# Kernel optimization log

Hardware: AMD Instinct MI355X
Metric: run time of the kernel (lower is better)

## Reference

```python
import jax, jax.numpy as jnp
import numpy as np

B, L, D = 4, 816, 2048
SEP = 768            # gemma (image+text) prefix length
P_LEN = 3            # proprio tokens inside the action-expert block
N, K, H = 8, 1, 256  # heads, kv heads (GQA), head dim
G = N // K
GEMMA_MLP, ACTION_MLP = 16384, 4096
SOFTCAP = 50.0
BIG_NEG = -2.3819763e38


def rms_norm(x, scale, eps=1e-6):
    var = jnp.mean(jnp.square(x.astype(jnp.float32)), axis=-1, keepdims=True)
    normed = x * jax.lax.rsqrt(var + eps)
    return (normed * (1.0 + scale)).astype(x.dtype)


def apply_rope(x, positions, max_wavelength=10_000):
    # x: [B, T, n, H], positions: [B, T]
    head_dim = x.shape[-1]
    freq_exp = (2.0 / head_dim) * jnp.arange(head_dim // 2, dtype=jnp.float32)
    timescale = max_wavelength ** freq_exp
    radians = positions[..., None].astype(jnp.float32) / timescale[None, None, :]
    radians = radians[..., None, :]  # [B, T, 1, H/2]
    sin, cos = jnp.sin(radians), jnp.cos(radians)
    x1, x2 = jnp.split(x, 2, axis=-1)
    return jnp.concatenate([x1 * cos - x2 * sin, x2 * cos + x1 * sin], axis=-1).astype(x.dtype)


def get_qkv(xn, positions, wq, wkv):
    # wq: [N, D, H], wkv: [2, K, D, H]
    q = jnp.einsum('btd,ndh->btnh', xn, wq)
    k = jnp.einsum('bsd,kdh->bskh', xn, wkv[0])
    v = jnp.einsum('bsd,kdh->bskh', xn, wkv[1])
    q = apply_rope(q, positions) * (H ** -0.5)  # query_pre_attn_norm='rsqrt_head_dim'
    k = apply_rope(k, positions)
    return q, k, v


def geglu_ffn(x, w_gating, w_linear):
    # gemma GeGLU: w_gating [2, D, hidden], w_linear [hidden, D]
    gate = jax.nn.gelu(jnp.einsum('btd,dh->bth', x, w_gating[0]))
    act = gate * jnp.einsum('btd,dh->bth', x, w_gating[1])
    return jnp.einsum('bth,hd->btd', act, w_linear)


def setup_inputs() -> dict:
    key = jax.random.key(0)
    ks = jax.random.split(key, 16)
    s = 0.02
    x = jax.random.normal(ks[0], (B, L, D), jnp.float32)
    positions = jnp.broadcast_to(jnp.arange(L, dtype=jnp.int32), (B, L))
    # PiZero block mask: full attention within gemma prefix; proprio and action
    # blocks attend to everything before them plus themselves (mask_ar cumsum trick).
    mask_ar = np.zeros(L, dtype=np.int64)
    mask_ar[SEP] = 1
    mask_ar[SEP + P_LEN] = 1
    cm = np.cumsum(mask_ar)
    attn = cm[None, :] <= cm[:, None]  # [L_q, L_kv]
    attn_mask = jnp.asarray(np.broadcast_to(attn[None, None], (B, 1, L, L)))
    return {
        'x': x,
        'positions': positions,
        'attn_mask': attn_mask,
        'separation_idx': SEP,
        'pre_attn_scale': jnp.zeros((D,), jnp.float32),
        'pre_ffw_scale': jnp.zeros((D,), jnp.float32),
        'gq_w': jax.random.normal(ks[1], (N, D, H), jnp.float32) * s,
        'gkv_w': jax.random.normal(ks[2], (2, K, D, H), jnp.float32) * s,
        'go_w': jax.random.normal(ks[3], (N, H, D), jnp.float32) * s,
        'aq_w': jax.random.normal(ks[4], (N, D, H), jnp.float32) * s,
        'akv_w': jax.random.normal(ks[5], (2, K, D, H), jnp.float32) * s,
        'ao_w': jax.random.normal(ks[6], (N, H, D), jnp.float32) * s,
        'g_gating': jax.random.normal(ks[7], (2, D, GEMMA_MLP), jnp.float32) * s,
        'g_linear': jax.random.normal(ks[8], (GEMMA_MLP, D), jnp.float32) * s,
        'a_gating': jax.random.normal(ks[9], (2, D, ACTION_MLP), jnp.float32) * s,
        'a_linear': jax.random.normal(ks[10], (ACTION_MLP, D), jnp.float32) * s,
    }


def reference(x, positions, attn_mask, separation_idx, pre_attn_scale, pre_ffw_scale,
              gq_w, gkv_w, go_w, aq_w, akv_w, ao_w,
              g_gating, g_linear, a_gating, a_linear):
    sep = separation_idx
    xg, xa = x[:, :sep, :], x[:, sep:, :]
    # shared pre-attention RMSNorm applied to both expert streams
    ng = rms_norm(xg, pre_attn_scale)
    na = rms_norm(xa, pre_attn_scale)
    pg, pa = positions[:, :sep], positions[:, sep:]
    qg, kg, vg = get_qkv(ng, pg, gq_w, gkv_w)
    qa, ka, va = get_qkv(na, pa, aq_w, akv_w)
    # joint attention over concatenated streams
    q = jnp.concatenate([qg, qa], axis=1)   # [B, L, N, H]
    k = jnp.concatenate([kg, ka], axis=1)   # [B, L, K, H]
    v = jnp.concatenate([vg, va], axis=1)
    Bq, T = q.shape[0], q.shape[1]
    qr = q.reshape(Bq, T, K, G, H)
    logits = jnp.einsum('btkgh,bskh->bkgts', qr, k)
    logits = jnp.tanh(logits / SOFTCAP) * SOFTCAP  # attn logit softcap
    logits = jnp.where(attn_mask[:, :, None, :, :], logits, BIG_NEG)
    probs = jax.nn.softmax(logits.astype(jnp.float32), axis=-1).astype(logits.dtype)
    attn_out = jnp.einsum('bkgts,bskh->btkgh', probs, v).reshape(Bq, T, N, H)
    # per-expert output projections
    og = jnp.einsum('btnh,nhd->btd', attn_out[:, :sep], go_w)
    oa = jnp.einsum('btnh,nhd->btd', attn_out[:, sep:], ao_w)

    def post(attn_o, res, gating, lin):
        # faithful to source: final residual is mlp(norm(attn+res)) + res
        h = rms_norm(attn_o + res, pre_ffw_scale)
        return geglu_ffn(h, gating, lin) + res

    yg = post(og, xg, g_gating, g_linear)
    ya = post(oa, xa, a_gating, a_linear)
    return jnp.concatenate([yg, ya], axis=1)
```

## Files before the change

### kernel.cpp

```cpp
#include <hip/hip_runtime.h>
#include <hip/hip_bf16.h>

typedef __bf16 bfx8 __attribute__((ext_vector_type(8)));
typedef __bf16 bfx4 __attribute__((ext_vector_type(4)));
typedef float f32x4 __attribute__((ext_vector_type(4)));

#define MFMA16(a, b, c) __builtin_amdgcn_mfma_f32_16x16x32_bf16((a), (b), (c), 0, 0, 0)

__device__ __forceinline__ void gl_lds16(const __bf16* g, __bf16* l) {
  __builtin_amdgcn_global_load_lds(
      (const __attribute__((address_space(1))) unsigned int*)(const void*)g,
      (__attribute__((address_space(3))) unsigned int*)(void*)l, 16, 0, 0);
}

__device__ __forceinline__ unsigned pack_bf2(float a, float b) {
  unsigned short ua = __builtin_bit_cast(unsigned short, (__bf16)a);
  unsigned short ub = __builtin_bit_cast(unsigned short, (__bf16)b);
  return (unsigned)ua | ((unsigned)ub << 16);
}

__device__ __forceinline__ float gelu_tanh_f(float x) {
  float u = 0.7978845608028654f * (x + 0.044715f * x * x * x);
  float t;
  if (u > 10.f) t = 1.f;
  else if (u < -10.f) t = -1.f;
  else { float e = __expf(2.f * u); t = (e - 1.f) / (e + 1.f); }
  return 0.5f * x * (1.f + t);
}

__global__ __launch_bounds__(256)
void rmsnorm_kernel(const float* __restrict__ X, const float* __restrict__ X2,
                    const float* __restrict__ scale, __bf16* __restrict__ out) {
  __shared__ float wsum[4];
  const int row = blockIdx.x, tid = threadIdx.x;
  const size_t base = (size_t)row * 2048;
  f32x4 v[2];
  float ss = 0.f;
#pragma unroll
  for (int i = 0; i < 2; ++i) {
    const int idx = tid * 4 + i * 1024;
    v[i] = *(const f32x4*)(X + base + idx);
    if (X2) { f32x4 u = *(const f32x4*)(X2 + base + idx); v[i] = v[i] + u; }
#pragma unroll
    for (int j = 0; j < 4; ++j) ss += v[i][j] * v[i][j];
  }
#pragma unroll
  for (int o = 32; o > 0; o >>= 1) ss += __shfl_xor(ss, o, 64);
  if ((tid & 63) == 0) wsum[tid >> 6] = ss;
  __syncthreads();
  const float tot = wsum[0] + wsum[1] + wsum[2] + wsum[3];
  const float rs = rsqrtf(tot * (1.f / 2048.f) + 1e-6f);
#pragma unroll
  for (int i = 0; i < 2; ++i) {
    const int idx = tid * 4 + i * 1024;
    f32x4 sc = *(const f32x4*)(scale + idx);
    bfx4 ov;
#pragma unroll
    for (int j = 0; j < 4; ++j) ov[j] = (__bf16)(v[i][j] * rs * (1.f + sc[j]));
    *(bfx4*)(out + base + idx) = ov;
  }
}

__global__ __launch_bounds__(256)
void rope_bf_kernel(__bf16* __restrict__ buf, const int* __restrict__ pos,
                    int nheads, int rstride, float outscale) {
  const int row = blockIdx.x;
  const float p = (float)pos[row];
  const int total = nheads * 128;
  const size_t rbase = (size_t)row * (size_t)rstride;
  for (int idx = threadIdx.x; idx < total; idx += 256) {
    const int n = idx >> 7, i = idx & 127;
    const float ts = __expf(-(float)i * 0.071955784f);
    float sn, cs;
    __sincosf(p * ts, &sn, &cs);
    __bf16* bp = buf + rbase + n * 256 + i;
    const float x1 = (float)bp[0], x2 = (float)bp[128];
    bp[0]   = (__bf16)((x1 * cs - x2 * sn) * outscale);
    bp[128] = (__bf16)((x2 * cs + x1 * sn) * outscale);
  }
}

__global__ __launch_bounds__(256)
void rope_kernel(const float* __restrict__ in, const int* __restrict__ pos,
                 __bf16* __restrict__ outp, int nheads, float outscale) {
  const int row = blockIdx.x;
  const float p = (float)pos[row];
  const int total = nheads * 128;
  const size_t rbase = (size_t)row * (size_t)(nheads * 256);
  for (int idx = threadIdx.x; idx < total; idx += 256) {
    const int n = idx >> 7, i = idx & 127;
    const float ts = __expf(-(float)i * 0.071955784f);
    float sn, cs;
    __sincosf(p * ts, &sn, &cs);
    const float* bp = in + rbase + n * 256 + i;
    const float x1 = bp[0], x2 = bp[128];
    __bf16* ob = outp + rbase + n * 256 + i;
    ob[0]   = (__bf16)((x1 * cs - x2 * sn) * outscale);
    ob[128] = (__bf16)((x2 * cs + x1 * sn) * outscale);
  }
}

__global__ __launch_bounds__(256)
void convw_kernel(const float* __restrict__ in, __bf16* __restrict__ out,
                  int K, int headDim) {
  __shared__ __bf16 tile[64][65];
  const int tc0 = blockIdx.x * 64;
  const int tk0 = blockIdx.y * 64;
  const int tid = threadIdx.x;
  const int cchunk = tid & 15, krow = tid >> 4;
  const int c = tc0 + cchunk * 4;
  const float* colbase = in + (size_t)(c / headDim) * (size_t)K * headDim + (c % headDim);
#pragma unroll
  for (int i = 0; i < 4; ++i) {
    const int k = tk0 + krow + i * 16;
    f32x4 v = *(const f32x4*)(colbase + (size_t)k * headDim);
#pragma unroll
    for (int j = 0; j < 4; ++j) tile[cchunk * 4 + j][krow + i * 16] = (__bf16)v[j];
  }
  __syncthreads();
  const int nks = K >> 5;
#pragma unroll
  for (int s = 0; s < 2; ++s) {
    const int ch = tid + s * 256;
    const int wc = ch >> 3, wk8 = (ch & 7) * 8;
    bfx8 v;
#pragma unroll
    for (int j = 0; j < 8; ++j) v[j] = tile[wc][wk8 + j];
    const int col = tc0 + wc;
    const int kchunk = (tk0 + wk8) >> 3;
    const int cp = col >> 7, m = col & 127;
    const int ks = kchunk >> 2, lg = kchunk & 3;
    const int p = lg ^ ((m >> 1) & 3);
    *(bfx8*)(out + ((size_t)(cp * nks + ks)) * 4096 + m * 32 + p * 8) = v;
  }
}

__global__ __launch_bounds__(512, 2)
void ffn_dual256(const __bf16* __restrict__ A, const __bf16* __restrict__ Wg,
                 const __bf16* __restrict__ Wa, __bf16* __restrict__ C,
                 int Mpb, int lda, int strideA, int Kd,
                 int ldc, int strideC, int mbPerBatch) {
  __shared__ __align__(16) __bf16 As[2 * 2 * 8192];
  __shared__ __align__(16) __bf16 Bs[2 * 2 * 8192];
  const int tid = threadIdx.x;
  const int lane = tid & 63;
  const int wid = tid >> 6;
  const int wr = wid >> 2;
  const int wc = wid & 3;
  const int qi = lane & 15, g = lane >> 4;
  const int b = blockIdx.x / mbPerBatch;
  const int row0 = (blockIdx.x % mbPerBatch) * 256;
  const int col0 = blockIdx.y * 128;
  const __bf16* Ab = A + (size_t)b * strideA;
  const size_t nks = (size_t)(Kd >> 5);
  const __bf16* Bgp = Wg + ((size_t)(col0 >> 7)) * nks * 4096;
  const __bf16* Bap = Wa + ((size_t)(col0 >> 7)) * nks * 4096;
  const int NT = Kd >> 6;

  const int sm = tid >> 2, sp = tid & 3;
  const int slg = sp ^ ((sm >> 1) & 3);
  int r0 = row0 + sm;       if (r0 >= Mpb) r0 = Mpb - 1;
  int r1 = row0 + 128 + sm; if (r1 >= Mpb) r1 = Mpb - 1;
  const __bf16* asrc0 = Ab + (size_t)r0 * lda + slg * 8;
  const __bf16* asrc1 = Ab + (size_t)r1 * lda + slg * 8;

  auto stage_half = [&](int gh) {
    if (gh >= 4 * NT) return;
    const int t = gh >> 2, which = gh & 3;
    const int bufi = t & 1;
    if ((which & 1) == 0) {
      const int h = which >> 1;
      __bf16* dst = &As[bufi * 16384 + h * 8192];
      const __bf16* src = (h ? asrc1 : asrc0) + t * 64;
      gl_lds16(src, dst + tid * 8);
      gl_lds16(src + 32, dst + 4096 + tid * 8);
    } else {
      const int pan = which >> 1;
      __bf16* dst = &Bs[bufi * 16384 + pan * 8192];
      const __bf16* src = (pan ? Bap : Bgp) + (size_t)(t * 2) * 4096 + tid * 8;
      gl_lds16(src, dst + tid * 8);
      gl_lds16(src + 4096, dst + 4096 + tid * 8);
    }
  };

  f32x4 acc[2][2][4][2];
#pragma unroll
  for (int a0 = 0; a0 < 2; ++a0)
#pragma unroll
    for (int a1 = 0; a1 < 2; ++a1)
#pragma unroll
      for (int a2 = 0; a2 < 4; ++a2)
#pragma unroll
        for (int a3 = 0; a3 < 2; ++a3) acc[a0][a1][a2][a3] = f32x4{0.f, 0.f, 0.f, 0.f};

  for (int gh = 0; gh < 6; ++gh) stage_half(gh);
  asm volatile("s_waitcnt vmcnt(4)" ::: "memory");
  __builtin_amdgcn_s_barrier();
  asm volatile("" ::: "memory");

  for (int t = 0; t < NT; ++t) {
    const int cb = (t & 1) * 16384;
    bfx8 af[4][2], bf[2][2][2];

#pragma unroll
    for (int mi = 0; mi < 4; ++mi) {
      const int m = wr * 64 + mi * 16 + qi;
      const int sl = g ^ ((m >> 1) & 3);
      const int ba = cb + m * 32 + sl * 8;
      af[mi][0] = *(const bfx8*)(&As[ba]);
      af[mi][1] = *(const bfx8*)(&As[ba + 4096]);
    }
#pragma unroll
    for (int pan = 0; pan < 2; ++pan)
#pragma unroll
      for (int ni = 0; ni < 2; ++ni) {
        const int m = wc * 32 + ni * 16 + qi;
        const int sl = g ^ ((m >> 1) & 3);
        const int bb = cb + pan * 8192 + m * 32 + sl * 8;
        bf[pan][ni][0] = *(const bfx8*)(&Bs[bb]);
        bf[pan][ni][1] = *(const bfx8*)(&Bs[bb + 4096]);
      }
    stage_half(4 * t + 6);
    stage_half(4 * t + 7);
    __builtin_amdgcn_s_barrier();
    asm volatile("s_waitcnt lgkmcnt(0)" ::: "memory");
    __builtin_amdgcn_sched_barrier(0);
    __builtin_amdgcn_s_setprio(1);
#pragma unroll
    for (int pan = 0; pan < 2; ++pan)
#pragma unroll
      for (int mi = 0; mi < 4; ++mi)
#pragma unroll
        for (int ni = 0; ni < 2; ++ni) {
          acc[0][pan][mi][ni] = MFMA16(af[mi][0], bf[pan][ni][0], acc[0][pan][mi][ni]);
          acc[0][pan][mi][ni] = MFMA16(af[mi][1], bf[pan][ni][1], acc[0][pan][mi][ni]);
        }
    __builtin_amdgcn_s_setprio(0);
    __builtin_amdgcn_s_barrier();
    asm volatile("" ::: "memory");

#pragma unroll
    for (int mi = 0; mi < 4; ++mi) {
      const int m = wr * 64 + mi * 16 + qi;
      const int sl = g ^ ((m >> 1) & 3);
      const int ba = cb + 8192 + m * 32 + sl * 8;
      af[mi][0] = *(const bfx8*)(&As[ba]);
      af[mi][1] = *(const bfx8*)(&As[ba + 4096]);
    }
    stage_half(4 * t + 8);
    stage_half(4 * t + 9);
    if (t + 2 < NT) asm volatile("s_waitcnt vmcnt(4)" ::: "memory");
    else            asm volatile("s_waitcnt vmcnt(0)" ::: "memory");
    __builtin_amdgcn_s_barrier();
    asm volatile("s_waitcnt lgkmcnt(0)" ::: "memory");
    __builtin_amdgcn_sched_barrier(0);
    __builtin_amdgcn_s_setprio(1);
#pragma unroll
    for (int pan = 0; pan < 2; ++pan)
#pragma unroll
      for (int mi = 0; mi < 4; ++mi)
#pragma unroll
        for (int ni = 0; ni < 2; ++ni) {
          acc[1][pan][mi][ni] = MFMA16(af[mi][0], bf[pan][ni][0], acc[1][pan][mi][ni]);
          acc[1][pan][mi][ni] = MFMA16(af[mi][1], bf[pan][ni][1], acc[1][pan][mi][ni]);
        }
    __builtin_amdgcn_s_setprio(0);
    __builtin_amdgcn_s_barrier();
    asm volatile("" ::: "memory");
  }

#pragma unroll
  for (int mh = 0; mh < 2; ++mh)
#pragma unroll
    for (int mi = 0; mi < 4; ++mi)
#pragma unroll
      for (int ni = 0; ni < 2; ++ni) {
        const int col = col0 + wc * 32 + ni * 16 + qi;
#pragma unroll
        for (int r = 0; r < 4; ++r) {
          const int row = row0 + mh * 128 + wr * 64 + mi * 16 + g * 4 + r;
          if (row >= Mpb) continue;
          C[(size_t)b * strideC + (size_t)row * ldc + col] =
              (__bf16)(gelu_tanh_f(acc[mh][0][mi][ni][r]) * acc[mh][1][mi][ni][r]);
        }
      }
}

__global__ __launch_bounds__(256, 2)
void gemm_bt2(const __bf16* __restrict__ A, const __bf16* __restrict__ Bt,
              void* __restrict__ C, void* __restrict__ C2, const void* __restrict__ Extra,
              int Mpb, int lda, int strideA, int Kd,
              int ldc, int strideC, int mbPerBatch,
              int outMode, int ldct) {
  __shared__ __align__(16) __bf16 As[2][8192];
  __shared__ __align__(16) __bf16 Bs[2][8192];
  const int tid = threadIdx.x;
  const int lane = tid & 63;
  const int wid = tid >> 6;
  const int b = blockIdx.x / mbPerBatch;
  const int row0 = (blockIdx.x % mbPerBatch) * 128;
  const int col0 = blockIdx.y * 128;
  const __bf16* Ab = A + (size_t)b * strideA;
  const size_t nks = (size_t)(Kd >> 5);
  const __bf16* Bpan0 = Bt + ((size_t)(col0 >> 7)) * nks * 4096;
  const int wm = (wid >> 1) * 64, wn = (wid & 1) * 64;
  const int qi = lane & 15, g = lane >> 4;

  const int m0 = tid >> 2, p0 = tid & 3;
  const int lg0 = p0 ^ ((m0 >> 1) & 3);
  const int m1 = m0 + 64;
  const int lg1 = p0 ^ ((m1 >> 1) & 3);
  int mr0 = row0 + m0; if (mr0 >= Mpb) mr0 = Mpb - 1;
  int mr1 = row0 + m1; if (mr1 >= Mpb) mr1 = Mpb - 1;
  const __bf16* asrc0 = Ab + (size_t)mr0 * lda + lg0 * 8;
  const __bf16* asrc1 = Ab + (size_t)mr1 * lda + lg1 * 8;
  const int nt = Kd >> 6;

  auto stage = [&](int t, int bufi) {
    const int k0 = t * 64;
    gl_lds16(asrc0 + k0, &As[bufi][tid * 8]);
    gl_lds16(asrc1 + k0, &As[bufi][(tid + 256) * 8]);
    gl_lds16(asrc0 + k0 + 32, &As[bufi][4096 + tid * 8]);
    gl_lds16(asrc1 + k0 + 32, &As[bufi][4096 + (tid + 256) * 8]);
    const __bf16* pb = Bpan0 + (size_t)(k0 >> 5) * 4096;
    gl_lds16(pb + tid * 8, &Bs[bufi][tid * 8]);
    gl_lds16(pb + (tid + 256) * 8, &Bs[bufi][(tid + 256) * 8]);
    gl_lds16(pb + 4096 + tid * 8, &Bs[bufi][4096 + tid * 8]);
    gl_lds16(pb + 4096 + (tid + 256) * 8, &Bs[bufi][4096 + (tid + 256) * 8]);
  };

  f32x4 acc[4][4];
#pragma unroll
  for (int i = 0; i < 4; ++i)
#pragma unroll
    for (int j = 0; j < 4; ++j) acc[i][j] = f32x4{0.f, 0.f, 0.f, 0.f};

  stage(0, 0);
  if (nt > 1) stage(1, 1);

  for (int t = 0; t < nt; ++t) {
    const int cur = t & 1;
    if (t + 1 < nt) asm volatile("s_waitcnt vmcnt(8)" ::: "memory");
    else            asm volatile("s_waitcnt vmcnt(0)" ::: "memory");
    __builtin_amdgcn_s_barrier();
    asm volatile("" ::: "memory");
#pragma unroll
    for (int ks = 0; ks < 2; ++ks) {
      bfx8 af[4], bf[4];
#pragma unroll
      for (int mi = 0; mi < 4; ++mi) {
        const int m = wm + mi * 16 + qi;
        const int sl = g ^ ((m >> 1) & 3);
        af[mi] = *(const bfx8*)(&As[cur][ks * 4096 + m * 32 + sl * 8]);
      }
#pragma unroll
      for (int ni = 0; ni < 4; ++ni) {
        const int n = wn + ni * 16 + qi;
        const int sl = g ^ ((n >> 1) & 3);
        bf[ni] = *(const bfx8*)(&Bs[cur][ks * 4096 + n * 32 + sl * 8]);
      }
#pragma unroll
      for (int mi = 0; mi < 4; ++mi)
#pragma unroll
        for (int ni = 0; ni < 4; ++ni)
          acc[mi][ni] = MFMA16(af[mi], bf[ni], acc[mi][ni]);
    }
    asm volatile("s_waitcnt lgkmcnt(0)" ::: "memory");
    __builtin_amdgcn_s_barrier();
    asm volatile("" ::: "memory");
    if (t + 2 < nt) stage(t + 2, cur);
  }

#pragma unroll
  for (int mi = 0; mi < 4; ++mi) {
#pragma unroll
    for (int ni = 0; ni < 4; ++ni) {
      const int col = col0 + wn + ni * 16 + qi;
      if (outMode == 5 && col >= 2304) {
        const int vcol = col - 2304;
        const int rowb = row0 + wm + mi * 16 + g * 4;
        if (rowb < Mpb) {
          bfx4 ov;
#pragma unroll
          for (int r = 0; r < 4; ++r) ov[r] = (__bf16)acc[mi][ni][r];
          *(bfx4*)((__bf16*)C2 + (size_t)b * (256 * 816) + (size_t)vcol * 816 + rowb) = ov;
        }
        continue;
      }
#pragma unroll
      for (int r = 0; r < 4; ++r) {
        const int row = row0 + wm + mi * 16 + g * 4 + r;
        if (row >= Mpb) continue;
        const float v = acc[mi][ni][r];
        if (outMode == 0) {
          ((float*)C)[(size_t)b * strideC + (size_t)row * ldc + col] = v;
        } else if (outMode == 1 || outMode == 5) {
          ((__bf16*)C)[(size_t)b * strideC + (size_t)row * ldc + col] = (__bf16)v;
        } else {
          const size_t ix = (size_t)b * strideC + (size_t)row * ldc + col;
          ((float*)C)[ix] = v + ((const float*)Extra)[ix];
        }
      }
    }
  }
  (void)ldct;
}

__global__ __launch_bounds__(256, 2)
void ffn_dual(const __bf16* __restrict__ A, const __bf16* __restrict__ Wg,
              const __bf16* __restrict__ Wa, __bf16* __restrict__ C,
              int Mpb, int lda, int strideA, int Kd,
              int ldc, int strideC, int mbPerBatch) {
  __shared__ __align__(16) __bf16 As[2][8192];
  __shared__ __align__(16) __bf16 Bs[2][8192];
  const int tid = threadIdx.x;
  const int lane = tid & 63;
  const int wid = tid >> 6;
  const int b = blockIdx.x / mbPerBatch;
  const int row0 = (blockIdx.x % mbPerBatch) * 128;
  const int col0 = blockIdx.y * 128;
  const __bf16* Ab = A + (size_t)b * strideA;
  const size_t nks = (size_t)(Kd >> 5);
  const int wm = (wid >> 1) * 64, wn = (wid & 1) * 64;
  const int qi = lane & 15, g = lane >> 4;

  const int m0 = tid >> 2, p0 = tid & 3;
  const int lg0 = p0 ^ ((m0 >> 1) & 3);
  const int m1 = m0 + 64;
  const int lg1 = p0 ^ ((m1 >> 1) & 3);
  int mr0 = row0 + m0; if (mr0 >= Mpb) mr0 = Mpb - 1;
  int mr1 = row0 + m1; if (mr1 >= Mpb) mr1 = Mpb - 1;
  const __bf16* asrc0 = Ab + (size_t)mr0 * lda + lg0 * 8;
  const __bf16* asrc1 = Ab + (size_t)mr1 * lda + lg1 * 8;
  const int nt = Kd >> 6;

  f32x4 gval[4][4];
  f32x4 acc[4][4];

// ... 193 lines not shown
  const int qt = blockIdx.x, hn = blockIdx.y, b = blockIdx.z;
  const int q0 = qt * 64;
  const int qi = lane & 15, g = lane >> 4;

  int qrow = q0 + wid * 16 + qi;
  if (qrow > 815) qrow = 815;
  const int cmq = (qrow >= 768) + (qrow >= 771);
  const __bf16* qrp = qp + (size_t)(b * 816 + qrow) * qstride + hn * 256 + g * 8;
  bfx8 qf[8];
#pragma unroll
  for (int kf = 0; kf < 8; ++kf) qf[kf] = *(const bfx8*)(qrp + kf * 32);

  f32x4 oacc[16];
#pragma unroll
  for (int i = 0; i < 16; ++i) oacc[i] = f32x4{0.f, 0.f, 0.f, 0.f};
  float den = 0.f;

  const int ntiles = (q0 + 63 < 768) ? 12 : 13;
  for (int t = 0; t < ntiles; ++t) {
    const int kv0 = t * 64;
#pragma unroll
    for (int mi = 0; mi < 4; ++mi) {
      f32x4 sac = f32x4{0.f, 0.f, 0.f, 0.f};
      int srow = kv0 + mi * 16 + qi;
      if (srow > 815) srow = 815;
      const __bf16* kp = kp0 + (size_t)(b * 816 + srow) * kstride + g * 8;
#pragma unroll
      for (int kf = 0; kf < 8; ++kf) {
        bfx8 a = *(const bfx8*)(kp + kf * 32);
        sac = MFMA16(a, qf[kf], sac);
      }
      float pv[4];
#pragma unroll
      for (int r = 0; r < 4; ++r) {
        const int s = kv0 + mi * 16 + g * 4 + r;
        const float l = sac[r];
        const float e2 = __expf(l * 0.04f);
        const float capped = 50.f * (e2 - 1.f) / (e2 + 1.f);
        const int cms = (s >= 768) + (s >= 771);
        const bool ok = (s < 816) && (cms <= cmq);
        const float p = ok ? __expf(capped) : 0.f;
        den += p;
        pv[r] = p;
      }
      const unsigned lo = pack_bf2(pv[0], pv[1]);
      const unsigned hi = pack_bf2(pv[2], pv[3]);
      const int slot = 2 * mi + (g >> 1);
      const int phys = slot ^ (qi & 7);
      char* pb = (char*)&Ps[wid][0] + qi * 128 + phys * 16 + (g & 1) * 8;
      *(unsigned*)(pb) = lo;
      *(unsigned*)(pb + 4) = hi;
    }
    asm volatile("s_waitcnt lgkmcnt(0)" ::: "memory");
    bfx8 pa[2];
#pragma unroll
    for (int k2 = 0; k2 < 2; ++k2) {
      const int sl = (k2 * 4 + g) ^ (qi & 7);
      pa[k2] = *(const bfx8*)((const char*)&Ps[wid][0] + qi * 128 + sl * 16);
    }
#pragma unroll
    for (int hf = 0; hf < 16; ++hf) {
      const int h = hf * 16 + qi;
#pragma unroll
      for (int k2 = 0; k2 < 2; ++k2) {
        int s0 = kv0 + k2 * 32 + g * 8;
        if (s0 > 808) s0 = 808;
        bfx8 vb = *(const bfx8*)(vt + ((size_t)(b * 256 + h)) * 816 + s0);
        oacc[hf] = MFMA16(pa[k2], vb, oacc[hf]);
      }
    }
    asm volatile("s_waitcnt lgkmcnt(0)" ::: "memory");
  }

  den += __shfl_xor(den, 16, 64);
  den += __shfl_xor(den, 32, 64);
  if (lane < 16) denw[wid][qi] = den;
  asm volatile("s_waitcnt lgkmcnt(0)" ::: "memory");
#pragma unroll
  for (int r = 0; r < 4; ++r) {
    const int qg = q0 + wid * 16 + g * 4 + r;
    if (qg >= 816) continue;
    const float di = 1.f / denw[wid][g * 4 + r];
#pragma unroll
    for (int hf = 0; hf < 16; ++hf) {
      ao[((size_t)(b * 816 + qg)) * 2048 + hn * 256 + hf * 16 + qi] =
          (__bf16)(oacc[hf][r] * di);
    }
  }
}

extern "C" void kernel_launch(void* const* d_in, const int* in_sizes, int n_in,
                              void* d_out, int out_size, void* d_ws, size_t ws_size,
                              hipStream_t stream) {
  (void)in_sizes; (void)n_in; (void)out_size;
  const float* x      = (const float*)d_in[0];
  const int*   pos    = (const int*)d_in[1];
  const float* s_attn = (const float*)d_in[4];
  const float* s_ffw  = (const float*)d_in[5];
  const float* gq     = (const float*)d_in[6];
  const float* gkv    = (const float*)d_in[7];
  const float* go     = (const float*)d_in[8];
  const float* aq     = (const float*)d_in[9];
  const float* akv    = (const float*)d_in[10];
  const float* aow    = (const float*)d_in[11];
  const float* gg     = (const float*)d_in[12];
  const float* gl     = (const float*)d_in[13];
  const float* ag     = (const float*)d_in[14];
  const float* al     = (const float*)d_in[15];
  float* outp = (float*)d_out;
  char* ws = (char*)d_ws;
  dim3 blk(256);

  const size_t NEED_BATCH = 577437696u;
  const size_t NEED_FAST  = 423297024u;

  if (ws_size >= NEED_FAST) {
    const bool batched = (ws_size >= NEED_BATCH);
    __bf16* wQKVg = (__bf16*)(ws + 0);
    __bf16* wQKVa = (__bf16*)(ws + 10485760);
    __bf16* goT = (__bf16*)(ws + 20971520);
    __bf16* aoT = (__bf16*)(ws + 29360128);
    __bf16* ggT = (__bf16*)(ws + 37748736);
    __bf16* glT = (__bf16*)(ws + 171966464);
    __bf16* agT = (__bf16*)(ws + 239075328);
    __bf16* alT = (__bf16*)(ws + 272629760);
    __bf16* xn   = (__bf16*)(ws + 289406976);
    __bf16* qkb  = (__bf16*)(ws + 302776320);
    __bf16* vt   = (__bf16*)(ws + 317816832);
    __bf16* aob  = (__bf16*)(ws + 319488000);
    float*  ob   = (float*)(ws + 332857344);
    __bf16* hb   = (__bf16*)(ws + 359596032);
    __bf16* gate  = (__bf16*)(ws + 372965376);
    __bf16* act   = (__bf16*)(ws + 398131200);
    __bf16* act4  = (__bf16*)(ws + 473628672);
    __bf16* actA4 = (__bf16*)(ws + 575864832);

    convw_kernel<<<dim3(32, 32), blk, 0, stream>>>(gq, wQKVg, 2048, 256);
    convw_kernel<<<dim3(4, 32), blk, 0, stream>>>(gkv, wQKVg + 16 * 64 * 4096, 2048, 256);
    convw_kernel<<<dim3(4, 32), blk, 0, stream>>>(gkv + 2048 * 256, wQKVg + 18 * 64 * 4096, 2048, 256);
    convw_kernel<<<dim3(32, 32), blk, 0, stream>>>(aq, wQKVa, 2048, 256);
    convw_kernel<<<dim3(4, 32), blk, 0, stream>>>(akv, wQKVa + 16 * 64 * 4096, 2048, 256);
    convw_kernel<<<dim3(4, 32), blk, 0, stream>>>(akv + 2048 * 256, wQKVa + 18 * 64 * 4096, 2048, 256);
    convw_kernel<<<dim3(32, 32), blk, 0, stream>>>(go, goT, 2048, 2048);
    convw_kernel<<<dim3(32, 32), blk, 0, stream>>>(aow, aoT, 2048, 2048);
    convw_kernel<<<dim3(256, 32), blk, 0, stream>>>(gg, ggT, 2048, 16384);
    convw_kernel<<<dim3(256, 32), blk, 0, stream>>>(gg + (size_t)2048 * 16384, ggT + (size_t)16384 * 2048, 2048, 16384);
    convw_kernel<<<dim3(32, 256), blk, 0, stream>>>(gl, glT, 16384, 2048);
    convw_kernel<<<dim3(64, 32), blk, 0, stream>>>(ag, agT, 2048, 4096);
    convw_kernel<<<dim3(64, 32), blk, 0, stream>>>(ag + (size_t)2048 * 4096, agT + (size_t)4096 * 2048, 2048, 4096);
    convw_kernel<<<dim3(32, 64), blk, 0, stream>>>(al, alT, 4096, 2048);

    rmsnorm_kernel<<<3264, blk, 0, stream>>>(x, nullptr, s_attn, xn);

    gemm_bt2<<<dim3(24, 20), blk, 0, stream>>>(xn, wQKVg, qkb, vt, nullptr,
        768, 2048, 816 * 2048, 2048, 2304, 816 * 2304, 6, 5, 0);
    gemm_bt2<<<dim3(4, 20), blk, 0, stream>>>(xn + 768 * 2048, wQKVa, qkb + 768 * 2304, vt + 768, nullptr,
        48, 2048, 816 * 2048, 2048, 2304, 816 * 2304, 1, 5, 0);

    rope_bf_kernel<<<3264, blk, 0, stream>>>(qkb, pos, 8, 2304, 0.0625f);
    rope_bf_kernel<<<3264, blk, 0, stream>>>(qkb + 2048, pos, 1, 2304, 1.0f);

    attn_kernel<<<dim3(13, 8, 4), blk, 0, stream>>>(qkb, qkb + 2048, vt, aob, 2304, 2304);

    gemm_bt2<<<dim3(24, 16), blk, 0, stream>>>(aob, goT, ob, nullptr, nullptr,
        768, 2048, 816 * 2048, 2048, 2048, 816 * 2048, 6, 0, 0);
    gemm_bt2<<<dim3(4, 16), blk, 0, stream>>>(aob + 768 * 2048, aoT, ob + 768 * 2048, nullptr, nullptr,
        48, 2048, 816 * 2048, 2048, 2048, 816 * 2048, 1, 0, 0);

    rmsnorm_kernel<<<3264, blk, 0, stream>>>(ob, x, s_ffw, hb);

    if (batched) {
      ffn_dual256<<<dim3(12, 128), dim3(512), 0, stream>>>(hb, ggT, ggT + (size_t)16384 * 2048, act4,
          768, 2048, 816 * 2048, 2048, 16384, 768 * 16384, 3);
      gemm_bt2<<<dim3(24, 16), blk, 0, stream>>>(act4, glT, outp, nullptr, x,
          768, 16384, 768 * 16384, 16384, 2048, 816 * 2048, 6, 2, 0);
      ffn_dual<<<dim3(4, 32), blk, 0, stream>>>(hb + 768 * 2048, agT, agT + (size_t)4096 * 2048, actA4,
          48, 2048, 816 * 2048, 2048, 4096, 48 * 4096, 1);
      gemm_bt2<<<dim3(4, 16), blk, 0, stream>>>(actA4, alT, outp + 768 * 2048, nullptr, x + 768 * 2048,
          48, 4096, 48 * 4096, 4096, 2048, 816 * 2048, 1, 2, 0);
    } else {
      for (int bb = 0; bb < 4; ++bb) {
        const __bf16* hg = hb + (size_t)bb * 816 * 2048;
        float* og = outp + (size_t)bb * 816 * 2048;
        const float* xg = x + (size_t)bb * 816 * 2048;
        ffn_dual<<<dim3(6, 128), blk, 0, stream>>>(hg, ggT, ggT + (size_t)16384 * 2048, act,
            768, 2048, 0, 2048, 16384, 0, 6);
        gemm_bt2<<<dim3(6, 16), blk, 0, stream>>>(act, glT, og, nullptr, xg,
            768, 16384, 0, 16384, 2048, 0, 6, 2, 0);
        const __bf16* ha = hg + 768 * 2048;
        ffn_dual<<<dim3(1, 32), blk, 0, stream>>>(ha, agT, agT + (size_t)4096 * 2048, gate,
            48, 2048, 0, 2048, 4096, 0, 1);
        gemm_bt2<<<dim3(1, 16), blk, 0, stream>>>(gate, alT, og + 768 * 2048, nullptr, xg + 768 * 2048,
            48, 4096, 0, 4096, 2048, 0, 1, 2, 0);
      }
    }
    return;
  }

  if (ws_size < 164000000u) return;
  __bf16* xn   = (__bf16*)(ws + 0);
  float*  qf   = (float*)(ws + 13369344);
  __bf16* qbb  = (__bf16*)(ws + 40108032);
  float*  kf   = (float*)(ws + 53477376);
  __bf16* kbb  = (__bf16*)(ws + 56819712);
  __bf16* vt   = (__bf16*)(ws + 58490880);
  __bf16* aob  = (__bf16*)(ws + 60162048);
  float*  ob   = (float*)(ws + 73531392);
  __bf16* hb   = (__bf16*)(ws + 100270080);
  __bf16* gate = (__bf16*)(ws + 113639424);
  __bf16* act  = (__bf16*)(ws + 138805248);

  rmsnorm_kernel<<<3264, blk, 0, stream>>>(x, nullptr, s_attn, xn);
  gemm_kernel<<<dim3(24, 16), blk, 0, stream>>>(xn, gq, qf, nullptr,
      768, 2048, 816 * 2048, 256, 256, 2048, 2048, 816 * 2048, 6, 0, 0);
  gemm_kernel<<<dim3(4, 16), blk, 0, stream>>>(xn + 768 * 2048, aq, qf + 768 * 2048, nullptr,
      48, 2048, 816 * 2048, 256, 256, 2048, 2048, 816 * 2048, 1, 0, 0);
  gemm_kernel<<<dim3(24, 2), blk, 0, stream>>>(xn, gkv, kf, nullptr,
      768, 2048, 816 * 2048, 256, 256, 2048, 256, 816 * 256, 6, 0, 0);
  gemm_kernel<<<dim3(4, 2), blk, 0, stream>>>(xn + 768 * 2048, akv, kf + 768 * 256, nullptr,
      48, 2048, 816 * 2048, 256, 256, 2048, 256, 816 * 256, 1, 0, 0);
  gemm_kernel<<<dim3(24, 2), blk, 0, stream>>>(xn, gkv + 2048 * 256, vt, nullptr,
      768, 2048, 816 * 2048, 256, 256, 2048, 0, 256 * 816, 6, 3, 816);
  gemm_kernel<<<dim3(4, 2), blk, 0, stream>>>(xn + 768 * 2048, akv + 2048 * 256, vt + 768, nullptr,
      48, 2048, 816 * 2048, 256, 256, 2048, 0, 256 * 816, 1, 3, 816);
  rope_kernel<<<3264, blk, 0, stream>>>(qf, pos, qbb, 8, 0.0625f);
  rope_kernel<<<3264, blk, 0, stream>>>(kf, pos, kbb, 1, 1.0f);
  attn_kernel<<<dim3(13, 8, 4), blk, 0, stream>>>(qbb, kbb, vt, aob, 2048, 256);
  gemm_kernel<<<dim3(24, 16), blk, 0, stream>>>(aob, go, ob, nullptr,
      768, 2048, 816 * 2048, 2048, 0, 2048, 2048, 816 * 2048, 6, 0, 0);
  gemm_kernel<<<dim3(4, 16), blk, 0, stream>>>(aob + 768 * 2048, aow, ob + 768 * 2048, nullptr,
      48, 2048, 816 * 2048, 2048, 0, 2048, 2048, 816 * 2048, 1, 0, 0);
  rmsnorm_kernel<<<3264, blk, 0, stream>>>(ob, x, s_ffw, hb);
  for (int bb = 0; bb < 4; ++bb) {
    const __bf16* hg = hb + (size_t)bb * 816 * 2048;
    float* og = outp + (size_t)bb * 816 * 2048;
    const float* xg = x + (size_t)bb * 816 * 2048;
    gemm_kernel<<<dim3(6, 128), blk, 0, stream>>>(hg, gg, gate, nullptr,
        768, 2048, 0, 16384, 0, 2048, 16384, 0, 6, 1, 0);
    gemm_kernel<<<dim3(6, 128), blk, 0, stream>>>(hg, gg + 2048 * 16384, act, gate,
        768, 2048, 0, 16384, 0, 2048, 16384, 0, 6, 4, 0);
    gemm_kernel<<<dim3(6, 16), blk, 0, stream>>>(act, gl, og, xg,
        768, 16384, 0, 2048, 0, 16384, 2048, 0, 6, 2, 0);
    const __bf16* ha = hg + 768 * 2048;
    gemm_kernel<<<dim3(1, 32), blk, 0, stream>>>(ha, ag, gate, nullptr,
        48, 2048, 0, 4096, 0, 2048, 4096, 0, 1, 1, 0);
    gemm_kernel<<<dim3(1, 32), blk, 0, stream>>>(ha, ag + 2048 * 4096, act, gate,
        48, 2048, 0, 4096, 0, 2048, 4096, 0, 1, 4, 0);
    gemm_kernel<<<dim3(1, 16), blk, 0, stream>>>(act, al, og + 768 * 2048, xg + 768 * 2048,
        48, 4096, 0, 2048, 0, 4096, 2048, 0, 1, 2, 0);
  }
}
```

Measured before the change: 1.423 ms.

## Add 256x128-tile 512-thread GEMM for large projections and XCD-aware block remap

Adds a gemm256 kernel with 256-row by 128-column tiles and 8 waves. It is used for the gemma QKV, output projection and down-projection GEMMs, so each B tile is reused across twice as many rows. Both gemm256 and ffn_dual256 remap workgroup ids in groups of 8 so that neighbouring tiles share an XCD and its L2. The cost is fewer workgroups (for example 192 on the output projection), which may underfill the CUs, and the loads are staged in finer pieces.

New measurement: 1.409 ms, median of 3. No clear change (-1.0%).

```diff
diff --git a/kernel.cpp b/kernel.cpp
--- a/kernel.cpp
+++ b/kernel.cpp
@@ -148,9 +148,13 @@
   const int wr = wid >> 2;
   const int wc = wid & 3;
   const int qi = lane & 15, g = lane >> 4;
-  const int b = blockIdx.x / mbPerBatch;
-  const int row0 = (blockIdx.x % mbPerBatch) * 256;
-  const int col0 = blockIdx.y * 128;
+  int bid = blockIdx.y * gridDim.x + blockIdx.x;
+  const int nwg = gridDim.x * gridDim.y;
+  if ((nwg & 7) == 0) bid = (bid & 7) * (nwg >> 3) + (bid >> 3);
+  const int bx = bid % gridDim.x, by = bid / gridDim.x;
+  const int b = bx / mbPerBatch;
+  const int row0 = (bx % mbPerBatch) * 256;
+  const int col0 = by * 128;
   const __bf16* Ab = A + (size_t)b * strideA;
   const size_t nks = (size_t)(Kd >> 5);
   const __bf16* Bgp = Wg + ((size_t)(col0 >> 7)) * nks * 4096;
@@ -282,6 +286,169 @@
           if (row >= Mpb) continue;
           C[(size_t)b * strideC + (size_t)row * ldc + col] =
               (__bf16)(gelu_tanh_f(acc[mh][0][mi][ni][r]) * acc[mh][1][mi][ni][r]);
+        }
+      }
+}
+
+__global__ __launch_bounds__(512, 2)
+void gemm256(const __bf16* __restrict__ A, const __bf16* __restrict__ Bt,
+             void* __restrict__ C, void* __restrict__ C2, const void* __restrict__ Extra,
+             int Mpb, int lda, int strideA, int Kd,
+             int ldc, int strideC, int mbPerBatch, int outMode) {
+  __shared__ __align__(16) __bf16 As[2 * 2 * 8192];
+  __shared__ __align__(16) __bf16 Bs[2 * 8192];
+  const int tid = threadIdx.x;
+  const int lane = tid & 63;
+  const int wid = tid >> 6;
+  const int wr = wid >> 2;
+  const int wc = wid & 3;
+  const int qi = lane & 15, g = lane >> 4;
+  int bid = blockIdx.y * gridDim.x + blockIdx.x;
+  const int nwg = gridDim.x * gridDim.y;
+  if ((nwg & 7) == 0) bid = (bid & 7) * (nwg >> 3) + (bid >> 3);
+  const int bx = bid % gridDim.x, by = bid / gridDim.x;
+  const int b = bx / mbPerBatch;
+  const int row0 = (bx % mbPerBatch) * 256;
+  const int col0 = by * 128;
+  const __bf16* Ab = A + (size_t)b * strideA;
+  const size_t nks = (size_t)(Kd >> 5);
+  const __bf16* Bp = Bt + ((size_t)(col0 >> 7)) * nks * 4096;
+  const int NT = Kd >> 6;
+
+  const int sm = tid >> 2, sp = tid & 3;
+  const int slg = sp ^ ((sm >> 1) & 3);
+  int r0 = row0 + sm;       if (r0 >= Mpb) r0 = Mpb - 1;
+  int r1 = row0 + 128 + sm; if (r1 >= Mpb) r1 = Mpb - 1;
+  const __bf16* asrc0 = Ab + (size_t)r0 * lda + slg * 8;
+  const __bf16* asrc1 = Ab + (size_t)r1 * lda + slg * 8;
+
+  auto stage_half = [&](int gh) {
+    if (gh >= 3 * NT) return;
+    const int t = gh / 3, which = gh - 3 * t;
+    const int bufi = t & 1;
+    if (which == 1) {
+      __bf16* dst = &Bs[bufi * 8192];
+      const __bf16* src = Bp + (size_t)(t * 2) * 4096 + tid * 8;
+      gl_lds16(src, dst + tid * 8);
+      gl_lds16(src + 4096, dst + 4096 + tid * 8);
+    } else {
+      const int h = which >> 1;
+      __bf16* dst = &As[bufi * 16384 + h * 8192];
+      const __bf16* src = (h ? asrc1 : asrc0) + t * 64;
+      gl_lds16(src, dst + tid * 8);
+      gl_lds16(src + 32, dst + 4096 + tid * 8);
+    }
+  };
+
+  f32x4 acc[2][4][2];
+#pragma unroll
+  for (int a0 = 0; a0 < 2; ++a0)
+#pragma unroll
+    for (int a2 = 0; a2 < 4; ++a2)
+#pragma unroll
+      for (int a3 = 0; a3 < 2; ++a3) acc[a0][a2][a3] = f32x4{0.f, 0.f, 0.f, 0.f};
+
+  for (int gh = 0; gh < 5; ++gh) stage_half(gh);
+  asm volatile("s_waitcnt vmcnt(4)" ::: "memory");
+  __builtin_amdgcn_s_barrier();
+  asm volatile("" ::: "memory");
+
+  for (int t = 0; t < NT; ++t) {
+    const int cb = (t & 1) * 16384;
+    const int cbB = (t & 1) * 8192;
+    bfx8 af[4][2], bf[2][2];
+
+#pragma unroll
+    for (int mi = 0; mi < 4; ++mi) {
+      const int m = wr * 64 + mi * 16 + qi;
+      const int sl = g ^ ((m >> 1) & 3);
+      const int ba = cb + m * 32 + sl * 8;
+      af[mi][0] = *(const bfx8*)(&As[ba]);
+      af[mi][1] = *(const bfx8*)(&As[ba + 4096]);
+    }
+#pragma unroll
+    for (int ni = 0; ni < 2; ++ni) {
+      const int m = wc * 32 + ni * 16 + qi;
+      const int sl = g ^ ((m >> 1) & 3);
+      const int bb = cbB + m * 32 + sl * 8;
+      bf[ni][0] = *(const bfx8*)(&Bs[bb]);
+      bf[ni][1] = *(const bfx8*)(&Bs[bb + 4096]);
+    }
+    stage_half(3 * t + 5);
+    __builtin_amdgcn_s_barrier();
+    asm volatile("s_waitcnt lgkmcnt(0)" ::: "memory");
+    __builtin_amdgcn_sched_barrier(0);
+    __builtin_amdgcn_s_setprio(1);
+#pragma unroll
+    for (int mi = 0; mi < 4; ++mi)
+#pragma unroll
+      for (int ni = 0; ni < 2; ++ni) {
+        acc[0][mi][ni] = MFMA16(af[mi][0], bf[ni][0], acc[0][mi][ni]);
+        acc[0][mi][ni] = MFMA16(af[mi][1], bf[ni][1], acc[0][mi][ni]);
+      }
+    __builtin_amdgcn_s_setprio(0);
+    __builtin_amdgcn_s_barrier();
+    asm volatile("" ::: "memory");
+
+#pragma unroll
+    for (int mi = 0; mi < 4; ++mi) {
+      const int m = wr * 64 + mi * 16 + qi;
+      const int sl = g ^ ((m >> 1) & 3);
+      const int ba = cb + 8192 + m * 32 + sl * 8;
+      af[mi][0] = *(const bfx8*)(&As[ba]);
+      af[mi][1] = *(const bfx8*)(&As[ba + 4096]);
+    }
+    stage_half(3 * t + 6);
+    stage_half(3 * t + 7);
+    if (t + 2 < NT) asm volatile("s_waitcnt vmcnt(4)" ::: "memory");
+    else            asm volatile("s_waitcnt vmcnt(0)" ::: "memory");
+    __builtin_amdgcn_s_barrier();
+    asm volatile("s_waitcnt lgkmcnt(0)" ::: "memory");
+    __builtin_amdgcn_sched_barrier(0);
+    __builtin_amdgcn_s_setprio(1);
+#pragma unroll
+    for (int mi = 0; mi < 4; ++mi)
+#pragma unroll
+      for (int ni = 0; ni < 2; ++ni) {
+        acc[1][mi][ni] = MFMA16(af[mi][0], bf[ni][0], acc[1][mi][ni]);
+        acc[1][mi][ni] = MFMA16(af[mi][1], bf[ni][1], acc[1][mi][ni]);
+      }
+    __builtin_amdgcn_s_setprio(0);
+    __builtin_amdgcn_s_barrier();
+    asm volatile("" ::: "memory");
+  }
+
+#pragma unroll
+  for (int mh = 0; mh < 2; ++mh)
+#pragma unroll
+    for (int mi = 0; mi < 4; ++mi)
+#pragma unroll
+      for (int ni = 0; ni < 2; ++ni) {
+        const int col = col0 + wc * 32 + ni * 16 + qi;
+        if (outMode == 5 && col >= 2304) {
+          const int vcol = col - 2304;
+          const int rowb = row0 + mh * 128 + wr * 64 + mi * 16 + g * 4;
+          if (rowb < Mpb) {
+            bfx4 ov;
+#pragma unroll
+            for (int r = 0; r < 4; ++r) ov[r] = (__bf16)acc[mh][mi][ni][r];
+            *(bfx4*)((__bf16*)C2 + (size_t)b * (256 * 816) + (size_t)vcol * 816 + rowb) = ov;
+          }
+          continue;
+        }
+#pragma unroll
+        for (int r = 0; r < 4; ++r) {
+          const int row = row0 + mh * 128 + wr * 64 + mi * 16 + g * 4 + r;
+          if (row >= Mpb) continue;
+          const float v = acc[mh][mi][ni][r];
+          if (outMode == 0) {
+            ((float*)C)[(size_t)b * strideC + (size_t)row * ldc + col] = v;
+          } else if (outMode == 5) {
+            ((__bf16*)C)[(size_t)b * strideC + (size_t)row * ldc + col] = (__bf16)v;
+          } else {
+            const size_t ix = (size_t)b * strideC + (size_t)row * ldc + col;
+            ((float*)C)[ix] = v + ((const float*)Extra)[ix];
+          }
         }
       }
 }
@@ -783,8 +950,8 @@
 
     rmsnorm_kernel<<<3264, blk, 0, stream>>>(x, nullptr, s_attn, xn);
 
-    gemm_bt2<<<dim3(24, 20), blk, 0, stream>>>(xn, wQKVg, qkb, vt, nullptr,
-        768, 2048, 816 * 2048, 2048, 2304, 816 * 2304, 6, 5, 0);
+    gemm256<<<dim3(12, 20), dim3(512), 0, stream>>>(xn, wQKVg, qkb, vt, nullptr,
+        768, 2048, 816 * 2048, 2048, 2304, 816 * 2304, 3, 5);
     gemm_bt2<<<dim3(4, 20), blk, 0, stream>>>(xn + 768 * 2048, wQKVa, qkb + 768 * 2304, vt + 768, nullptr,
         48, 2048, 816 * 2048, 2048, 2304, 816 * 2304, 1, 5, 0);
 
@@ -793,8 +960,8 @@
 
     attn_kernel<<<dim3(13, 8, 4), blk, 0, stream>>>(qkb, qkb + 2048, vt, aob, 2304, 2304);
 
-    gemm_bt2<<<dim3(24, 16), blk, 0, stream>>>(aob, goT, ob, nullptr, nullptr,
-        768, 2048, 816 * 2048, 2048, 2048, 816 * 2048, 6, 0, 0);
+    gemm256<<<dim3(12, 16), dim3(512), 0, stream>>>(aob, goT, ob, nullptr, nullptr,
+        768, 2048, 816 * 2048, 2048, 2048, 816 * 2048, 3, 0);
     gemm_bt2<<<dim3(4, 16), blk, 0, stream>>>(aob + 768 * 2048, aoT, ob + 768 * 2048, nullptr, nullptr,
         48, 2048, 816 * 2048, 2048, 2048, 816 * 2048, 1, 0, 0);
 
@@ -803,8 +970,8 @@
     if (batched) {
       ffn_dual256<<<dim3(12, 128), dim3(512), 0, stream>>>(hb, ggT, ggT + (size_t)16384 * 2048, act4,
           768, 2048, 816 * 2048, 2048, 16384, 768 * 16384, 3);
-      gemm_bt2<<<dim3(24, 16), blk, 0, stream>>>(act4, glT, outp, nullptr, x,
-          768, 16384, 768 * 16384, 16384, 2048, 816 * 2048, 6, 2, 0);
+      gemm256<<<dim3(12, 16), dim3(512), 0, stream>>>(act4, glT, outp, nullptr, x,
+          768, 16384, 768 * 16384, 16384, 2048, 816 * 2048, 3, 2);
       ffn_dual<<<dim3(4, 32), blk, 0, stream>>>(hb + 768 * 2048, agT, agT + (size_t)4096 * 2048, actA4,
           48, 2048, 816 * 2048, 2048, 4096, 48 * 4096, 1);
       gemm_bt2<<<dim3(4, 16), blk, 0, stream>>>(actA4, alT, outp + 768 * 2048, nullptr, x + 768 * 2048,
```

## Generalize 256x256 dual-panel kernel to QKV, out-proj and FFN-down GEMMs

Applied to the files above, without the earlier changes.

The FFN gate/up kernel is turned into a general dual-panel kernel with a 256x256 output tile made of two adjacent 128-column panels. Its epilogue gains output modes for plain fp32, fp32 plus residual, and bf16 with a transposed V store. The gemma QKV, attention-output and FFN-down projections now use it instead of the 128x128 gemm_bt2, which raises data reuse per block. It also adds a block-index remap that groups blocks in strides of eight. The trade-off is far fewer blocks (for example 96 or 120) on a many-CU GPU, which may leave compute units idle.

New measurement: 1.554 ms. +9.2%, slower.

```diff
diff --git a/kernel.cpp b/kernel.cpp
--- a/kernel.cpp
+++ b/kernel.cpp
@@ -136,10 +136,11 @@
 }
 
 __global__ __launch_bounds__(512, 2)
-void ffn_dual256(const __bf16* __restrict__ A, const __bf16* __restrict__ Wg,
-                 const __bf16* __restrict__ Wa, __bf16* __restrict__ C,
-                 int Mpb, int lda, int strideA, int Kd,
-                 int ldc, int strideC, int mbPerBatch) {
+void dual256(const __bf16* __restrict__ A, const __bf16* __restrict__ W0,
+             const __bf16* __restrict__ W1, void* __restrict__ C,
+             void* __restrict__ C2, const void* __restrict__ Extra,
+             int Mpb, int lda, int strideA, int Kd,
+             int ldc, int strideC, int mbPerBatch, int outMode) {
   __shared__ __align__(16) __bf16 As[2 * 2 * 8192];
   __shared__ __align__(16) __bf16 Bs[2 * 2 * 8192];
   const int tid = threadIdx.x;
@@ -148,13 +149,18 @@
   const int wr = wid >> 2;
   const int wc = wid & 3;
   const int qi = lane & 15, g = lane >> 4;
-  const int b = blockIdx.x / mbPerBatch;
-  const int row0 = (blockIdx.x % mbPerBatch) * 256;
-  const int col0 = blockIdx.y * 128;
+  int bid = blockIdx.y * gridDim.x + blockIdx.x;
+  const int nwg = gridDim.x * gridDim.y;
+  if ((nwg & 7) == 0) bid = (bid & 7) * (nwg >> 3) + (bid >> 3);
+  const int bx = bid % gridDim.x, by = bid / gridDim.x;
+  const int b = bx / mbPerBatch;
+  const int row0 = (bx % mbPerBatch) * 256;
+  const int colw = (outMode == 4) ? 128 : 256;
+  const int col0 = by * colw;
   const __bf16* Ab = A + (size_t)b * strideA;
   const size_t nks = (size_t)(Kd >> 5);
-  const __bf16* Bgp = Wg + ((size_t)(col0 >> 7)) * nks * 4096;
-  const __bf16* Bap = Wa + ((size_t)(col0 >> 7)) * nks * 4096;
+  const __bf16* Bgp = W0 + ((size_t)(col0 >> 7)) * nks * 4096;
+  const __bf16* Bap = W1 + ((size_t)(col0 >> 7)) * nks * 4096;
   const int NT = Kd >> 6;
 
   const int sm = tid >> 2, sp = tid & 3;
@@ -269,21 +275,59 @@
     asm volatile("" ::: "memory");
   }
 
-#pragma unroll
-  for (int mh = 0; mh < 2; ++mh)
-#pragma unroll
-    for (int mi = 0; mi < 4; ++mi)
-#pragma unroll
-      for (int ni = 0; ni < 2; ++ni) {
-        const int col = col0 + wc * 32 + ni * 16 + qi;
-#pragma unroll
-        for (int r = 0; r < 4; ++r) {
-          const int row = row0 + mh * 128 + wr * 64 + mi * 16 + g * 4 + r;
-          if (row >= Mpb) continue;
-          C[(size_t)b * strideC + (size_t)row * ldc + col] =
-              (__bf16)(gelu_tanh_f(acc[mh][0][mi][ni][r]) * acc[mh][1][mi][ni][r]);
+  if (outMode == 4) {
+#pragma unroll
+    for (int mh = 0; mh < 2; ++mh)
+#pragma unroll
+      for (int mi = 0; mi < 4; ++mi)
+#pragma unroll
+        for (int ni = 0; ni < 2; ++ni) {
+          const int col = col0 + wc * 32 + ni * 16 + qi;
+#pragma unroll
+          for (int r = 0; r < 4; ++r) {
+            const int row = row0 + mh * 128 + wr * 64 + mi * 16 + g * 4 + r;
+            if (row >= Mpb) continue;
+            ((__bf16*)C)[(size_t)b * strideC + (size_t)row * ldc + col] =
+                (__bf16)(gelu_tanh_f(acc[mh][0][mi][ni][r]) * acc[mh][1][mi][ni][r]);
+          }
         }
-      }
+  } else {
+#pragma unroll
+    for (int mh = 0; mh < 2; ++mh)
+#pragma unroll
+      for (int pan = 0; pan < 2; ++pan)
+#pragma unroll
+        for (int mi = 0; mi < 4; ++mi)
+#pragma unroll
+          for (int ni = 0; ni < 2; ++ni) {
+            const int col = col0 + pan * 128 + wc * 32 + ni * 16 + qi;
+            if (outMode == 5 && col >= 2304) {
+              const int vcol = col - 2304;
+              const int rowb = row0 + mh * 128 + wr * 64 + mi * 16 + g * 4;
+              if (rowb < Mpb) {
+                bfx4 ov;
+#pragma unroll
+                for (int r = 0; r < 4; ++r) ov[r] = (__bf16)acc[mh][pan][mi][ni][r];
+                *(bfx4*)((__bf16*)C2 + (size_t)b * (256 * 816) + (size_t)vcol * 816 + rowb) = ov;
+              }
+              continue;
+            }
+#pragma unroll
+            for (int r = 0; r < 4; ++r) {
+              const int row = row0 + mh * 128 + wr * 64 + mi * 16 + g * 4 + r;
+              if (row >= Mpb) continue;
+              const float v = acc[mh][pan][mi][ni][r];
+              if (outMode == 0) {
+                ((float*)C)[(size_t)b * strideC + (size_t)row * ldc + col] = v;
+              } else if (outMode == 5) {
+                ((__bf16*)C)[(size_t)b * strideC + (size_t)row * ldc + col] = (__bf16)v;
+              } else {
+                const size_t ix = (size_t)b * strideC + (size_t)row * ldc + col;
+                ((float*)C)[ix] = v + ((const float*)Extra)[ix];
+              }
+            }
+          }
+  }
 }
 
 __global__ __launch_bounds__(256, 2)
@@ -783,8 +827,8 @@
 
     rmsnorm_kernel<<<3264, blk, 0, stream>>>(x, nullptr, s_attn, xn);
 
-    gemm_bt2<<<dim3(24, 20), blk, 0, stream>>>(xn, wQKVg, qkb, vt, nullptr,
-        768, 2048, 816 * 2048, 2048, 2304, 816 * 2304, 6, 5, 0);
+    dual256<<<dim3(12, 10), dim3(512), 0, stream>>>(xn, wQKVg, wQKVg + 64 * 4096, qkb, vt, nullptr,
+        768, 2048, 816 * 2048, 2048, 2304, 816 * 2304, 3, 5);
     gemm_bt2<<<dim3(4, 20), blk, 0, stream>>>(xn + 768 * 2048, wQKVa, qkb + 768 * 2304, vt + 768, nullptr,
         48, 2048, 816 * 2048, 2048, 2304, 816 * 2304, 1, 5, 0);
 
@@ -793,18 +837,18 @@
 
     attn_kernel<<<dim3(13, 8, 4), blk, 0, stream>>>(qkb, qkb + 2048, vt, aob, 2304, 2304);
 
-    gemm_bt2<<<dim3(24, 16), blk, 0, stream>>>(aob, goT, ob, nullptr, nullptr,
-        768, 2048, 816 * 2048, 2048, 2048, 816 * 2048, 6, 0, 0);
+    dual256<<<dim3(12, 8), dim3(512), 0, stream>>>(aob, goT, goT + 64 * 4096, ob, nullptr, nullptr,
+        768, 2048, 816 * 2048, 2048, 2048, 816 * 2048, 3, 0);
     gemm_bt2<<<dim3(4, 16), blk, 0, stream>>>(aob + 768 * 2048, aoT, ob + 768 * 2048, nullptr, nullptr,
         48, 2048, 816 * 2048, 2048, 2048, 816 * 2048, 1, 0, 0);
 
     rmsnorm_kernel<<<3264, blk, 0, stream>>>(ob, x, s_ffw, hb);
 
     if (batched) {
-      ffn_dual256<<<dim3(12, 128), dim3(512), 0, stream>>>(hb, ggT, ggT + (size_t)16384 * 2048, act4,
-          768, 2048, 816 * 2048, 2048, 16384, 768 * 16384, 3);
-      gemm_bt2<<<dim3(24, 16), blk, 0, stream>>>(act4, glT, outp, nullptr, x,
-          768, 16384, 768 * 16384, 16384, 2048, 816 * 2048, 6, 2, 0);
+      dual256<<<dim3(12, 128), dim3(512), 0, stream>>>(hb, ggT, ggT + (size_t)16384 * 2048, act4, nullptr, nullptr,
+          768, 2048, 816 * 2048, 2048, 16384, 768 * 16384, 3, 4);
+      dual256<<<dim3(12, 8), dim3(512), 0, stream>>>(act4, glT, glT + 512 * 4096, outp, nullptr, x,
+          768, 16384, 768 * 16384, 16384, 2048, 816 * 2048, 3, 2);
       ffn_dual<<<dim3(4, 32), blk, 0, stream>>>(hb + 768 * 2048, agT, agT + (size_t)4096 * 2048, actA4,
           48, 2048, 816 * 2048, 2048, 4096, 48 * 4096, 1);
       gemm_bt2<<<dim3(4, 16), blk, 0, stream>>>(actA4, alT, outp + 768 * 2048, nullptr, x + 768 * 2048,
```
